# Kernel optimization log

Measured on AMD Instinct MI355X. Metric: run time of the kernel, lower is better.

## Reference

```python
import jax, jax.numpy as jnp
import numpy as np

NEG_SLOPE = 0.2
BN_EPS = 1e-5


def gat_conv(x, src, dst, W, att_src, att_dst, bias):
    """PyG-style GATConv (eval mode, shared src/dst lin, self-loops already in src/dst)."""
    N = x.shape[0]
    H, C = att_src.shape
    h = (x @ W).reshape(N, H, C)                      # [N,H,C]
    a_s = jnp.sum(h * att_src[None], axis=-1)         # [N,H]
    a_d = jnp.sum(h * att_dst[None], axis=-1)         # [N,H]
    e = jax.nn.leaky_relu(a_s[src] + a_d[dst], NEG_SLOPE)   # [E,H]
    # segment softmax over edges grouped by destination node
    m = jax.ops.segment_max(e, dst, num_segments=N)   # [N,H]
    ee = jnp.exp(e - m[dst])
    denom = jax.ops.segment_sum(ee, dst, num_segments=N)
    alpha = ee / (denom[dst] + 1e-16)                 # [E,H]
    msg = h[src] * alpha[..., None]                   # [E,H,C]
    out = jax.ops.segment_sum(msg, dst, num_segments=N)  # [N,H,C]
    return out.reshape(N, H * C) + bias


def setup_inputs() -> dict:
    key = jax.random.key(0)
    ks = jax.random.split(key, 12)
    N, E, Fin, C1, H, Fout = 50000, 800000, 128, 16, 8, 40
    HC = H * C1
    x = jax.random.normal(ks[0], (N, Fin), jnp.float32)
    edge_index = jax.random.randint(ks[1], (2, E), 0, N, dtype=jnp.int32)
    W1 = jax.random.normal(ks[2], (Fin, HC), jnp.float32) / np.sqrt(Fin).astype(np.float32)
    att_src1 = jax.random.normal(ks[3], (H, C1), jnp.float32) * 0.1
    att_dst1 = jax.random.normal(ks[4], (H, C1), jnp.float32) * 0.1
    b1 = jnp.zeros((HC,), jnp.float32)
    bn_gamma = jnp.ones((HC,), jnp.float32)
    bn_beta = jnp.zeros((HC,), jnp.float32)
    bn_mean = jnp.zeros((HC,), jnp.float32)
    bn_var = jnp.ones((HC,), jnp.float32)
    W2 = jax.random.normal(ks[5], (HC, Fout), jnp.float32) / np.sqrt(HC).astype(np.float32)
    att_src2 = jax.random.normal(ks[6], (1, Fout), jnp.float32) * 0.1
    att_dst2 = jax.random.normal(ks[7], (1, Fout), jnp.float32) * 0.1
    b2 = jnp.zeros((Fout,), jnp.float32)
    return {"x": x, "edge_index": edge_index, "W1": W1, "att_src1": att_src1,
            "att_dst1": att_dst1, "b1": b1, "bn_gamma": bn_gamma, "bn_beta": bn_beta,
            "bn_mean": bn_mean, "bn_var": bn_var, "W2": W2, "att_src2": att_src2,
            "att_dst2": att_dst2, "b2": b2}


def reference(x, edge_index, W1, att_src1, att_dst1, b1, bn_gamma, bn_beta,
              bn_mean, bn_var, W2, att_src2, att_dst2, b2):
    N = x.shape[0]
    loop = jnp.arange(N, dtype=edge_index.dtype)
    src = jnp.concatenate([edge_index[0], loop])   # PyG add_self_loops=True
    dst = jnp.concatenate([edge_index[1], loop])
    h = gat_conv(x, src, dst, W1, att_src1, att_dst1, b1)
    h = (h - bn_mean) * jax.lax.rsqrt(bn_var + BN_EPS) * bn_gamma + bn_beta  # BN eval
    h = jax.nn.elu(h)
    out = gat_conv(h, src, dst, W2, att_src2, att_dst2, b2)
    return jax.nn.log_softmax(out, axis=1)
```

## Files before the change

### kernel.cpp

```cpp
#include <hip/hip_runtime.h>
#include <hip/hip_bf16.h>
#include <math.h>

#define LRELU(v) ((v) > 0.f ? (v) : 0.2f * (v))

typedef __attribute__((ext_vector_type(8))) short bf16x8;
typedef __attribute__((ext_vector_type(4))) float f32x4;

__device__ inline unsigned int f2bf(float f) {
  unsigned int u = __float_as_uint(f);
  return (u + 0x7fffu + ((u >> 16) & 1u)) >> 16;
}
__device__ inline float bf_lo(unsigned int u) { return __uint_as_float(u << 16); }
__device__ inline float bf_hi(unsigned int u) { return __uint_as_float(u & 0xffff0000u); }

__global__ __launch_bounds__(256) void wtrans_k(const float* __restrict__ W,
                                                unsigned short* __restrict__ wt)
{
  int idx = blockIdx.x * 256 + threadIdx.x;
  int k = idx >> 7, c = idx & 127;
  wt[c * 128 + k] = (unsigned short)f2bf(W[idx]);
}

#define LDA 152
__global__ __launch_bounds__(256) void gemm1_k(
    const float* __restrict__ x, const unsigned short* __restrict__ wt,
    const float* __restrict__ atts, const float* __restrict__ attd,
    unsigned short* __restrict__ h1s, float* __restrict__ as1,
    float* __restrict__ ad1, int N)
{
  __shared__ unsigned short xs[64 * LDA];
  const int t = threadIdx.x;
  const int row0 = blockIdx.x * 64;
  const int lane = t & 63, w = t >> 6;

#pragma unroll
  for (int i = 0; i < 8; ++i) {
    int idx = t + i * 256;
    int r = idx >> 5, kq = idx & 31;
    int rr = row0 + r;
    float4 v = make_float4(0.f, 0.f, 0.f, 0.f);
    if (rr < N) v = *reinterpret_cast<const float4*>(&x[(size_t)rr * 128 + kq * 4]);
    unsigned int p0 = f2bf(v.x) | (f2bf(v.y) << 16);
    unsigned int p1 = f2bf(v.z) | (f2bf(v.w) << 16);
    *reinterpret_cast<uint2*>(&xs[r * LDA + kq * 4]) = make_uint2(p0, p1);
  }
  __syncthreads();

  const int l16 = lane & 15, lhi = lane >> 4;
  const int nb0 = w * 32;
  f32x4 acc[4][2];
#pragma unroll
  for (int m = 0; m < 4; ++m)
#pragma unroll
    for (int n = 0; n < 2; ++n) acc[m][n] = (f32x4){0.f, 0.f, 0.f, 0.f};

#pragma unroll
  for (int ks = 0; ks < 4; ++ks) {
    bf16x8 bf[2];
#pragma unroll
    for (int n = 0; n < 2; ++n) {
      int col = nb0 + n * 16 + l16;
      bf[n] = *reinterpret_cast<const bf16x8*>(&wt[col * 128 + ks * 32 + 8 * lhi]);
    }
#pragma unroll
    for (int m = 0; m < 4; ++m) {
      bf16x8 af = *reinterpret_cast<const bf16x8*>(
          &xs[(m * 16 + l16) * LDA + ks * 32 + 8 * lhi]);
      acc[m][0] = __builtin_amdgcn_mfma_f32_16x16x32_bf16(af, bf[0], acc[m][0], 0, 0, 0);
      acc[m][1] = __builtin_amdgcn_mfma_f32_16x16x32_bf16(af, bf[1], acc[m][1], 0, 0, 0);
    }
  }

#pragma unroll
  for (int n = 0; n < 2; ++n) {
    int col = nb0 + n * 16 + l16;
    float av = atts[col], dv = attd[col];
    int head = w * 2 + n;
#pragma unroll
    for (int m = 0; m < 4; ++m) {
#pragma unroll
      for (int r = 0; r < 4; ++r) {
        int row = row0 + m * 16 + lhi * 4 + r;
        float v = acc[m][n][r];
        float s = v * av, d = v * dv;
        s += __shfl_xor(s, 1); s += __shfl_xor(s, 2);
        s += __shfl_xor(s, 4); s += __shfl_xor(s, 8);
        d += __shfl_xor(d, 1); d += __shfl_xor(d, 2);
        d += __shfl_xor(d, 4); d += __shfl_xor(d, 8);
        if (row < N) {
          h1s[(size_t)row * 128 + col] = (unsigned short)f2bf(v);
          if (l16 == 0) { as1[row * 8 + head] = s; ad1[row * 8 + head] = d; }
        }
      }
    }
  }
}

#define NBUK_MAX 256

__global__ __launch_bounds__(256) void bhist_k(const int* __restrict__ ei,
                                               int E, int N,
                                               int* __restrict__ bcnt, int nbuk)
{
  __shared__ int h[NBUK_MAX];
  for (int i = threadIdx.x; i < nbuk; i += 256) h[i] = 0;
  __syncthreads();
  const int Etot = E + N;
  const int base = blockIdx.x * 4096;
#pragma unroll 4
  for (int i = threadIdx.x; i < 4096; i += 256) {
    int e = base + i;
    if (e < Etot) {
      int d = (e < E) ? ei[E + e] : (e - E);
      atomicAdd(&h[d >> 8], 1);
    }
  }
  __syncthreads();
  for (int i = threadIdx.x; i < nbuk; i += 256)
    if (h[i]) atomicAdd(&bcnt[i], h[i]);
}

__global__ __launch_bounds__(256) void bscan_k(const int* __restrict__ bcnt,
                                               int* __restrict__ bbase,
                                               int* __restrict__ bpos, int nbuk)
{
  __shared__ int wsum[4], wtot[4];
  const int t = threadIdx.x, lane = t & 63, w = t >> 6;
  int v = (t < nbuk) ? bcnt[t] : 0;
  int incl = v;
#pragma unroll
  for (int off = 1; off < 64; off <<= 1) {
    int y = __shfl_up(incl, off);
    if (lane >= off) incl += y;
  }
  if (lane == 63) wtot[w] = incl;
  __syncthreads();
  if (t == 0) {
    int a = wtot[0], b = wtot[1], c = wtot[2];
    wsum[0] = 0; wsum[1] = a; wsum[2] = a + b; wsum[3] = a + b + c;
  }
  __syncthreads();
  int ex = wsum[w] + incl - v;
  if (t < nbuk) { bbase[t] = ex; bpos[t] = ex; }
  if (t == nbuk - 1) bbase[nbuk] = ex + v;
}

__global__ __launch_bounds__(256) void bscat_k(const int* __restrict__ ei,
                                               int E, int N,
                                               int* __restrict__ bpos,
                                               unsigned int* __restrict__ stg,
                                               int nbuk)
{
  __shared__ int h[NBUK_MAX], gp[NBUK_MAX], cur[NBUK_MAX];
  for (int i = threadIdx.x; i < nbuk; i += 256) { h[i] = 0; cur[i] = 0; }
  __syncthreads();
  const int Etot = E + N;
  const int base = blockIdx.x * 4096;
  int s[16], d[16];
#pragma unroll
  for (int i = 0; i < 16; ++i) {
    int e = base + i * 256 + threadIdx.x;
    if (e < Etot) {
      if (e < E) { s[i] = ei[e]; d[i] = ei[E + e]; }
      else       { s[i] = d[i] = e - E; }
      atomicAdd(&h[d[i] >> 8], 1);
    } else d[i] = -1;
  }
  __syncthreads();
  for (int i = threadIdx.x; i < nbuk; i += 256)
    gp[i] = h[i] ? atomicAdd(&bpos[i], h[i]) : 0;
  __syncthreads();
#pragma unroll
  for (int i = 0; i < 16; ++i) {
    if (d[i] >= 0) {
      int b = d[i] >> 8;
      int r = atomicAdd(&cur[b], 1);
      stg[gp[b] + r] = ((unsigned int)s[i] << 8) | (unsigned int)(d[i] & 255);
    }
  }
}

#define CCAP 4992
__global__ __launch_bounds__(512) void csr_k(const unsigned int* __restrict__ stg,
                                             const int* __restrict__ bbase,
                                             int* __restrict__ rowptr,
                                             int* __restrict__ col,
                                             int N, int nbuk)
{
  __shared__ int nh[256], nb[257], cur[256], wsum[4];
  __shared__ int cstage[CCAP];
  const int b = blockIdx.x, t = threadIdx.x;
  const int n0 = b << 8;
  const int e0 = bbase[b], e1 = bbase[b + 1], cnt = e1 - e0;
  if (t < 256) { nh[t] = 0; cur[t] = 0; }
  __syncthreads();
  for (int i = t; i < cnt; i += 512)
    atomicAdd(&nh[stg[e0 + i] & 255u], 1);
  __syncthreads();
  if (t < 256) {
    const int lane = t & 63, w = t >> 6;
    int v = nh[t], incl = v;
#pragma unroll
    for (int off = 1; off < 64; off <<= 1) {
      int y = __shfl_up(incl, off);
      if (lane >= off) incl += y;
    }
    if (lane == 63) wsum[w] = incl;
    __syncthreads();
    if (t == 0) {
      int a = wsum[0], bb = wsum[1], c = wsum[2];
      wsum[0] = 0; wsum[1] = a; wsum[2] = a + bb; wsum[3] = a + bb + c;
    }
    __syncthreads();
    int ex = wsum[w] + incl - v;
    nb[t] = ex;
    if (t == 255) nb[256] = ex + v;
  } else {
    __syncthreads();
    __syncthreads();
  }
  __syncthreads();
  const int nnodes = min(256, N - n0);
  for (int i = t; i < nnodes; i += 512) rowptr[n0 + i] = e0 + nb[i];
  if (b == nbuk - 1 && t == 0) rowptr[N] = e1;
  for (int i = t; i < cnt; i += 512) {
    unsigned int sd = stg[e0 + i];
    int li = sd & 255u;
    int p = nb[li] + atomicAdd(&cur[li], 1);
    int sv = (int)(sd >> 8);
    if (p < CCAP) cstage[p] = sv; else col[e0 + p] = sv;
  }
  __syncthreads();
  const int lim = min(cnt, CCAP);
  for (int i = t; i < lim; i += 512) col[e0 + i] = cstage[i];
}

__global__ __launch_bounds__(256) void agg1_k(
    const unsigned int* __restrict__ h1b, const float* __restrict__ as1,
    const float* __restrict__ ad1, const int* __restrict__ rowptr,
    const int* __restrict__ col, const float* __restrict__ b1,
    const float* __restrict__ gamma, const float* __restrict__ beta,
    const float* __restrict__ mean, const float* __restrict__ var,
    float* __restrict__ hmid, int N)
{
  const int wid = threadIdx.x >> 6, lane = threadIdx.x & 63;
  const int n = blockIdx.x * 4 + wid;
  if (n >= N) return;
  const int eh = lane >> 5;
  const int cl = lane & 31;
  const int h  = cl >> 2;
  const float adv = ad1[n * 8 + h];
  float den = 0.f, a0 = 0.f, a1 = 0.f, a2 = 0.f, a3 = 0.f;
  const int jb = rowptr[n], je = rowptr[n + 1];
  for (int j = jb; j < je; j += 8) {
    int s[4]; bool v[4];
#pragma unroll
    for (int q = 0; q < 4; ++q) {
      int idx = j + 2 * q + eh;
      v[q] = idx < je;
      s[q] = col[v[q] ? idx : je - 1];
    }
    float e[4];
#pragma unroll
    for (int q = 0; q < 4; ++q) e[q] = as1[s[q] * 8 + h];
    uint2 u[4];
#pragma unroll
    for (int q = 0; q < 4; ++q)
      u[q] = *reinterpret_cast<const uint2*>(&h1b[s[q] * 64 + cl * 2]);
#pragma unroll
    for (int q = 0; q < 4; ++q) {
      float p = v[q] ? __expf(LRELU(e[q] + adv)) : 0.f;
      den += p;
      a0 += p * bf_lo(u[q].x);
      a1 += p * bf_hi(u[q].x);
      a2 += p * bf_lo(u[q].y);
      a3 += p * bf_hi(u[q].y);
    }
  }
  den += __shfl_xor(den, 32);
  a0 += __shfl_xor(a0, 32);
  a1 += __shfl_xor(a1, 32);
  a2 += __shfl_xor(a2, 32);
  a3 += __shfl_xor(a3, 32);
  if (eh == 0) {
    const int c0 = cl * 4;
    float r = 1.f / (den + 1e-16f);
    float4 bb = *reinterpret_cast<const float4*>(&b1[c0]);
    float4 mm = *reinterpret_cast<const float4*>(&mean[c0]);
    float4 vv = *reinterpret_cast<const float4*>(&var[c0]);
    float4 gg = *reinterpret_cast<const float4*>(&gamma[c0]);
    float4 be = *reinterpret_cast<const float4*>(&beta[c0]);
    float o0 = a0 * r + bb.x, o1 = a1 * r + bb.y;
    float o2 = a2 * r + bb.z, o3 = a3 * r + bb.w;
    float n0 = (o0 - mm.x) * rsqrtf(vv.x + 1e-5f) * gg.x + be.x;
    float n1 = (o1 - mm.y) * rsqrtf(vv.y + 1e-5f) * gg.y + be.y;
    float n2 = (o2 - mm.z) * rsqrtf(vv.z + 1e-5f) * gg.z + be.z;
    float n3 = (o3 - mm.w) * rsqrtf(vv.w + 1e-5f) * gg.w + be.w;
    float4 o;
    o.x = n0 > 0.f ? n0 : expm1f(n0);
    o.y = n1 > 0.f ? n1 : expm1f(n1);
    o.z = n2 > 0.f ? n2 : expm1f(n2);
    o.w = n3 > 0.f ? n3 : expm1f(n3);
    *reinterpret_cast<float4*>(&hmid[n * 128 + c0]) = o;
  }
}

__global__ __launch_bounds__(256) void gemm2_k(
    const float* __restrict__ hmid, const float* __restrict__ W2,
    const float* __restrict__ atts, const float* __restrict__ attd,
    float* __restrict__ h2p, float* __restrict__ as2, float* __restrict__ ad2,
    int N)
{
  __shared__ float hm[128 * 36];
  __shared__ float w2t[40 * 36];
  const int t = threadIdx.x;
  const int n0 = blockIdx.x * 128;
  const int lane = t & 63, w = t >> 6;
  const int ng = lane >> 3, cg = lane & 7;
  const int nloc = w * 32 + ng * 4;

  float acc[4][5];
#pragma unroll
  for (int i = 0; i < 4; ++i)
#pragma unroll
    for (int j = 0; j < 5; ++j) acc[i][j] = 0.f;

  for (int kc = 0; kc < 4; ++kc) {
    __syncthreads();
#pragma unroll
    for (int i = 0; i < 4; ++i) {
      int idx = t + i * 256;
      int r = idx >> 3, kq = idx & 7;
      int rr = n0 + r;
      float4 v = make_float4(0.f, 0.f, 0.f, 0.f);
      if (rr < N)
        v = *reinterpret_cast<const float4*>(&hmid[(size_t)rr * 128 + kc * 32 + kq * 4]);
      *reinterpret_cast<float4*>(&hm[r * 36 + kq * 4]) = v;
    }
#pragma unroll
    for (int i = 0; i < 5; ++i) {
      int flat = t + i * 256;
      int c = flat >> 5, kk = flat & 31;
      w2t[c * 36 + kk] = W2[(size_t)(kc * 32 + kk) * 40 + c];
    }
    __syncthreads();
#pragma unroll
    for (int k4 = 0; k4 < 8; ++k4) {
      float hv[4][4];
#pragma unroll
      for (int i = 0; i < 4; ++i)
        *reinterpret_cast<float4*>(hv[i]) =
            *reinterpret_cast<const float4*>(&hm[(nloc + i) * 36 + k4 * 4]);
      float wv[5][4];
#pragma unroll
      for (int j = 0; j < 5; ++j)
        *reinterpret_cast<float4*>(wv[j]) =
            *reinterpret_cast<const float4*>(&w2t[(cg * 5 + j) * 36 + k4 * 4]);
#pragma unroll
      for (int i = 0; i < 4; ++i)
#pragma unroll
        for (int j = 0; j < 5; ++j)
#pragma unroll
          for (int kk = 0; kk < 4; ++kk)
            acc[i][j] += hv[i][kk] * wv[j][kk];
    }
  }

  float asv[5], adv[5];
#pragma unroll
  for (int j = 0; j < 5; ++j) { asv[j] = atts[cg * 5 + j]; adv[j] = attd[cg * 5 + j]; }
#pragma unroll
  for (int i = 0; i < 4; ++i) {
    int n = n0 + nloc + i;
    if (n >= N) continue;
    float ps = 0.f, pd = 0.f;
#pragma unroll
    for (int j = 0; j < 5; ++j) { ps += acc[i][j] * asv[j]; pd += acc[i][j] * adv[j]; }
#pragma unroll
    for (int off = 1; off < 8; off <<= 1) {
      ps += __shfl_xor(ps, off);
      pd += __shfl_xor(pd, off);
    }
#pragma unroll
    for (int j = 0; j < 5; ++j) h2p[(size_t)n * 40 + cg * 5 + j] = acc[i][j];
    if (cg == 0) { as2[n] = ps; ad2[n] = pd; }
  }
}

__global__ __launch_bounds__(256) void agg2_k(
    const float* __restrict__ h2p, const float* __restrict__ as2,
    const float* __restrict__ ad2, const int* __restrict__ rowptr,
    const int* __restrict__ col, const float* __restrict__ b2,
    float* __restrict__ out, int N)
{
  const int wid = threadIdx.x >> 6, lane = threadIdx.x & 63;
  const int n = blockIdx.x * 4 + wid;
  if (n >= N) return;
  const int eh = lane >> 5;
  const int cl = lane & 31;
  const bool actc = cl < 20;
  const int c0 = (actc ? cl : 19) * 2;
  const float adv = ad2[n];
  float den = 0.f, a0 = 0.f, a1 = 0.f;
  const int jb = rowptr[n], je = rowptr[n + 1];
  for (int j = jb; j < je; j += 8) {
    int s[4]; bool v[4];
#pragma unroll
    for (int q = 0; q < 4; ++q) {
      int idx = j + 2 * q + eh;
      v[q] = idx < je;
      s[q] = col[v[q] ? idx : je - 1];
    }
    float e[4];
#pragma unroll
    for (int q = 0; q < 4; ++q) e[q] = as2[s[q]];
    float2 f[4];
#pragma unroll
    for (int q = 0; q < 4; ++q)
      f[q] = *reinterpret_cast<const float2*>(&h2p[s[q] * 40 + c0]);
#pragma unroll
    for (int q = 0; q < 4; ++q) {
      float p = v[q] ? __expf(LRELU(e[q] + adv)) : 0.f;
      den += p;
      a0 += p * f[q].x;
      a1 += p * f[q].y;
    }
  }
  den += __shfl_xor(den, 32);
  a0 += __shfl_xor(a0, 32);
  a1 += __shfl_xor(a1, 32);
  float r = 1.f / (den + 1e-16f);
  float o0 = a0 * r + b2[c0];
  float o1 = a1 * r + b2[c0 + 1];
  const bool act = actc && (eh == 0);
  float mv = act ? fmaxf(o0, o1) : -INFINITY;
#pragma unroll
  for (int off = 1; off < 32; off <<= 1) mv = fmaxf(mv, __shfl_xor(mv, off));
  float ex = act ? (__expf(o0 - mv) + __expf(o1 - mv)) : 0.f;
#pragma unroll
  for (int off = 1; off < 32; off <<= 1) ex += __shfl_xor(ex, off);
  float ls = logf(ex);
  if (act) {
    float2 ov = make_float2(o0 - mv - ls, o1 - mv - ls);
    *reinterpret_cast<float2*>(&out[n * 40 + c0]) = ov;
  }
}

extern "C" void kernel_launch(void* const* d_in, const int* in_sizes, int n_in,
                              void* d_out, int out_size, void* d_ws,
                              size_t ws_size, hipStream_t stream)
{
  const float* x      = (const float*)d_in[0];
  const int*   ei     = (const int*)d_in[1];
  const float* W1     = (const float*)d_in[2];
  const float* att_s1 = (const float*)d_in[3];
  const float* att_d1 = (const float*)d_in[4];
  const float* b1     = (const float*)d_in[5];
  const float* gamma  = (const float*)d_in[6];
  const float* beta   = (const float*)d_in[7];
  const float* mean   = (const float*)d_in[8];
  const float* var    = (const float*)d_in[9];
  const float* W2     = (const float*)d_in[10];
  const float* att_s2 = (const float*)d_in[11];
  const float* att_d2 = (const float*)d_in[12];
  const float* b2     = (const float*)d_in[13];
  float* out = (float*)d_out;

  const int N = in_sizes[0] / 128;
  const int E = in_sizes[1] / 2;
  const int Etot = E + N;
  const int nbuk = (N + 255) >> 8;
  const int nchunk = (Etot + 4095) / 4096;

  char* ws = (char*)d_ws;
  size_t off = 0;
  auto alloc = [&](size_t bytes) -> void* {
    void* p = ws + off;
    off = (off + bytes + 255) & ~(size_t)255;
    return p;
  };
  unsigned short* h1s = (unsigned short*)alloc((size_t)N * 128 * 2);
  float* as1  = (float*)alloc((size_t)N * 8 * 4);
  float* ad1  = (float*)alloc((size_t)N * 8 * 4);
  float* hmid = (float*)alloc((size_t)N * 128 * 4);
  int* rowptr = (int*)alloc((size_t)(N + 1) * 4);
  int* col    = (int*)alloc((size_t)Etot * 4);
  unsigned int* stg = (unsigned int*)alloc((size_t)Etot * 4);
  int* bcnt   = (int*)alloc(NBUK_MAX * 4);
  int* bbase  = (int*)alloc((NBUK_MAX + 1) * 4);
  int* bpos   = (int*)alloc(NBUK_MAX * 4);
  unsigned short* wt = (unsigned short*)alloc(16384 * 2);
  float* h2p = (float*)h1s;
  float* as2 = as1;
  float* ad2 = ad1;

  hipMemsetAsync(bcnt, 0, NBUK_MAX * 4, stream);

  wtrans_k<<<64, 256, 0, stream>>>(W1, wt);
  gemm1_k<<<(N + 63) / 64, 256, 0, stream>>>(x, wt, att_s1, att_d1,
                                             h1s, as1, ad1, N);
  bhist_k<<<nchunk, 256, 0, stream>>>(ei, E, N, bcnt, nbuk);
  bscan_k<<<1, 256, 0, stream>>>(bcnt, bbase, bpos, nbuk);
  bscat_k<<<nchunk, 256, 0, stream>>>(ei, E, N, bpos, stg, nbuk);
  csr_k<<<nbuk, 512, 0, stream>>>(stg, bbase, rowptr, col, N, nbuk);

  agg1_k<<<(N + 3) / 4, 256, 0, stream>>>((const unsigned int*)h1s, as1, ad1,
                                          rowptr, col, b1,
                                          gamma, beta, mean, var, hmid, N);
  gemm2_k<<<(N + 127) / 128, 256, 0, stream>>>(hmid, W2, att_s2, att_d2,
                                               h2p, as2, ad2, N);
  agg2_k<<<(N + 3) / 4, 256, 0, stream>>>(h2p, as2, ad2, rowptr, col, b2,
                                          out, N);
}
```

Measured before the change: 167.4 us.

## Fuse layer-2 linear projection into layer-1 aggregation kernel

Merges the first-layer attention aggregation with BN/ELU and the second-layer 128x40 projection into one kernel, keeping each node's 128-wide hidden row in shared memory instead of writing and re-reading a full hmid buffer. Each 4-node block stages all of W2 into LDS and computes the projection with a per-wave dot-product and shuffle reduction. This removes one kernel launch and a large global round-trip, but adds per-block W2 loads and more LDS use, and output buffers can no longer alias the layer-1 buffers.

```diff
diff --git a/kernel.cpp b/kernel.cpp
--- a/kernel.cpp
+++ b/kernel.cpp
@@ -236,155 +236,118 @@
   for (int i = t; i < lim; i += 512) col[e0 + i] = cstage[i];
 }
 
-__global__ __launch_bounds__(256) void agg1_k(
+__global__ __launch_bounds__(256) void agg1f_k(
     const unsigned int* __restrict__ h1b, const float* __restrict__ as1,
     const float* __restrict__ ad1, const int* __restrict__ rowptr,
     const int* __restrict__ col, const float* __restrict__ b1,
     const float* __restrict__ gamma, const float* __restrict__ beta,
     const float* __restrict__ mean, const float* __restrict__ var,
-    float* __restrict__ hmid, int N)
-{
-  const int wid = threadIdx.x >> 6, lane = threadIdx.x & 63;
-  const int n = blockIdx.x * 4 + wid;
-  if (n >= N) return;
-  const int eh = lane >> 5;
-  const int cl = lane & 31;
-  const int h  = cl >> 2;
-  const float adv = ad1[n * 8 + h];
-  float den = 0.f, a0 = 0.f, a1 = 0.f, a2 = 0.f, a3 = 0.f;
-  const int jb = rowptr[n], je = rowptr[n + 1];
-  for (int j = jb; j < je; j += 8) {
-    int s[4]; bool v[4];
-#pragma unroll
-    for (int q = 0; q < 4; ++q) {
-      int idx = j + 2 * q + eh;
-      v[q] = idx < je;
-      s[q] = col[v[q] ? idx : je - 1];
-    }
-    float e[4];
-#pragma unroll
-    for (int q = 0; q < 4; ++q) e[q] = as1[s[q] * 8 + h];
-    uint2 u[4];
-#pragma unroll
-    for (int q = 0; q < 4; ++q)
-      u[q] = *reinterpret_cast<const uint2*>(&h1b[s[q] * 64 + cl * 2]);
-#pragma unroll
-    for (int q = 0; q < 4; ++q) {
-      float p = v[q] ? __expf(LRELU(e[q] + adv)) : 0.f;
-      den += p;
-      a0 += p * bf_lo(u[q].x);
-      a1 += p * bf_hi(u[q].x);
-      a2 += p * bf_lo(u[q].y);
-      a3 += p * bf_hi(u[q].y);
-    }
-  }
-  den += __shfl_xor(den, 32);
-  a0 += __shfl_xor(a0, 32);
-  a1 += __shfl_xor(a1, 32);
-  a2 += __shfl_xor(a2, 32);
-  a3 += __shfl_xor(a3, 32);
-  if (eh == 0) {
-    const int c0 = cl * 4;
-    float r = 1.f / (den + 1e-16f);
-    float4 bb = *reinterpret_cast<const float4*>(&b1[c0]);
-    float4 mm = *reinterpret_cast<const float4*>(&mean[c0]);
-    float4 vv = *reinterpret_cast<const float4*>(&var[c0]);
-    float4 gg = *reinterpret_cast<const float4*>(&gamma[c0]);
-    float4 be = *reinterpret_cast<const float4*>(&beta[c0]);
-    float o0 = a0 * r + bb.x, o1 = a1 * r + bb.y;
-    float o2 = a2 * r + bb.z, o3 = a3 * r + bb.w;
-    float n0 = (o0 - mm.x) * rsqrtf(vv.x + 1e-5f) * gg.x + be.x;
-    float n1 = (o1 - mm.y) * rsqrtf(vv.y + 1e-5f) * gg.y + be.y;
-    float n2 = (o2 - mm.z) * rsqrtf(vv.z + 1e-5f) * gg.z + be.z;
-    float n3 = (o3 - mm.w) * rsqrtf(vv.w + 1e-5f) * gg.w + be.w;
-    float4 o;
-    o.x = n0 > 0.f ? n0 : expm1f(n0);
-    o.y = n1 > 0.f ? n1 : expm1f(n1);
-    o.z = n2 > 0.f ? n2 : expm1f(n2);
-    o.w = n3 > 0.f ? n3 : expm1f(n3);
-    *reinterpret_cast<float4*>(&hmid[n * 128 + c0]) = o;
-  }
-}
-
-__global__ __launch_bounds__(256) void gemm2_k(
-    const float* __restrict__ hmid, const float* __restrict__ W2,
-    const float* __restrict__ atts, const float* __restrict__ attd,
+    const float* __restrict__ W2, const float* __restrict__ atts2,
+    const float* __restrict__ attd2,
     float* __restrict__ h2p, float* __restrict__ as2, float* __restrict__ ad2,
     int N)
 {
-  __shared__ float hm[128 * 36];
-  __shared__ float w2t[40 * 36];
+  __shared__ float w2s[128 * 40];
+  __shared__ float hm[4 * 128];
   const int t = threadIdx.x;
-  const int n0 = blockIdx.x * 128;
-  const int lane = t & 63, w = t >> 6;
-  const int ng = lane >> 3, cg = lane & 7;
-  const int nloc = w * 32 + ng * 4;
-
-  float acc[4][5];
-#pragma unroll
-  for (int i = 0; i < 4; ++i)
-#pragma unroll
-    for (int j = 0; j < 5; ++j) acc[i][j] = 0.f;
-
-  for (int kc = 0; kc < 4; ++kc) {
-    __syncthreads();
-#pragma unroll
-    for (int i = 0; i < 4; ++i) {
-      int idx = t + i * 256;
-      int r = idx >> 3, kq = idx & 7;
-      int rr = n0 + r;
-      float4 v = make_float4(0.f, 0.f, 0.f, 0.f);
-      if (rr < N)
-        v = *reinterpret_cast<const float4*>(&hmid[(size_t)rr * 128 + kc * 32 + kq * 4]);
-      *reinterpret_cast<float4*>(&hm[r * 36 + kq * 4]) = v;
-    }
-#pragma unroll
-    for (int i = 0; i < 5; ++i) {
-      int flat = t + i * 256;
-      int c = flat >> 5, kk = flat & 31;
-      w2t[c * 36 + kk] = W2[(size_t)(kc * 32 + kk) * 40 + c];
-    }
-    __syncthreads();
-#pragma unroll
-    for (int k4 = 0; k4 < 8; ++k4) {
-      float hv[4][4];
-#pragma unroll
-      for (int i = 0; i < 4; ++i)
-        *reinterpret_cast<float4*>(hv[i]) =
-            *reinterpret_cast<const float4*>(&hm[(nloc + i) * 36 + k4 * 4]);
-      float wv[5][4];
-#pragma unroll
-      for (int j = 0; j < 5; ++j)
-        *reinterpret_cast<float4*>(wv[j]) =
-            *reinterpret_cast<const float4*>(&w2t[(cg * 5 + j) * 36 + k4 * 4]);
-#pragma unroll
-      for (int i = 0; i < 4; ++i)
-#pragma unroll
-        for (int j = 0; j < 5; ++j)
-#pragma unroll
-          for (int kk = 0; kk < 4; ++kk)
-            acc[i][j] += hv[i][kk] * wv[j][kk];
-    }
-  }
-
-  float asv[5], adv[5];
-#pragma unroll
-  for (int j = 0; j < 5; ++j) { asv[j] = atts[cg * 5 + j]; adv[j] = attd[cg * 5 + j]; }
-#pragma unroll
-  for (int i = 0; i < 4; ++i) {
-    int n = n0 + nloc + i;
-    if (n >= N) continue;
-    float ps = 0.f, pd = 0.f;
-#pragma unroll
-    for (int j = 0; j < 5; ++j) { ps += acc[i][j] * asv[j]; pd += acc[i][j] * adv[j]; }
-#pragma unroll
-    for (int off = 1; off < 8; off <<= 1) {
-      ps += __shfl_xor(ps, off);
-      pd += __shfl_xor(pd, off);
-    }
-#pragma unroll
-    for (int j = 0; j < 5; ++j) h2p[(size_t)n * 40 + cg * 5 + j] = acc[i][j];
-    if (cg == 0) { as2[n] = ps; ad2[n] = pd; }
+  const int wid = t >> 6, lane = t & 63;
+  const int n = blockIdx.x * 4 + wid;
+  const bool valid = n < N;
+
+  for (int i = t; i < 128 * 40; i += 256) w2s[i] = W2[i];
+
+  if (valid) {
+    const int eh = lane >> 5;
+    const int cl = lane & 31;
+    const int h  = cl >> 2;
+    const int c0 = cl * 4;
+    const float adv = ad1[n * 8 + h];
+    float den = 0.f, a0 = 0.f, a1 = 0.f, a2 = 0.f, a3 = 0.f;
+    const int jb = rowptr[n], je = rowptr[n + 1];
+    for (int j = jb; j < je; j += 8) {
+      int s[4]; bool v[4];
+#pragma unroll
+      for (int q = 0; q < 4; ++q) {
+        int idx = j + 2 * q + eh;
+        v[q] = idx < je;
+        s[q] = col[v[q] ? idx : je - 1];
+      }
+      float e[4];
+#pragma unroll
+      for (int q = 0; q < 4; ++q) e[q] = as1[s[q] * 8 + h];
+      uint2 u[4];
+#pragma unroll
+      for (int q = 0; q < 4; ++q)
+        u[q] = *reinterpret_cast<const uint2*>(&h1b[s[q] * 64 + cl * 2]);
+#pragma unroll
+      for (int q = 0; q < 4; ++q) {
+        float p = v[q] ? __expf(LRELU(e[q] + adv)) : 0.f;
+        den += p;
+        a0 += p * bf_lo(u[q].x);
+        a1 += p * bf_hi(u[q].x);
+        a2 += p * bf_lo(u[q].y);
+        a3 += p * bf_hi(u[q].y);
+      }
+    }
+    den += __shfl_xor(den, 32);
+    a0 += __shfl_xor(a0, 32);
+    a1 += __shfl_xor(a1, 32);
+    a2 += __shfl_xor(a2, 32);
+    a3 += __shfl_xor(a3, 32);
+    if (eh == 0) {
+      float r = 1.f / (den + 1e-16f);
+      float4 bb = *reinterpret_cast<const float4*>(&b1[c0]);
+      float4 mm = *reinterpret_cast<const float4*>(&mean[c0]);
+      float4 vv = *reinterpret_cast<const float4*>(&var[c0]);
+      float4 gg = *reinterpret_cast<const float4*>(&gamma[c0]);
+      float4 be = *reinterpret_cast<const float4*>(&beta[c0]);
+      float o0 = a0 * r + bb.x, o1 = a1 * r + bb.y;
+      float o2 = a2 * r + bb.z, o3 = a3 * r + bb.w;
+      float n0 = (o0 - mm.x) * rsqrtf(vv.x + 1e-5f) * gg.x + be.x;
+      float n1 = (o1 - mm.y) * rsqrtf(vv.y + 1e-5f) * gg.y + be.y;
+      float n2 = (o2 - mm.z) * rsqrtf(vv.z + 1e-5f) * gg.z + be.z;
+      float n3 = (o3 - mm.w) * rsqrtf(vv.w + 1e-5f) * gg.w + be.w;
+      float4 o;
+      o.x = n0 > 0.f ? n0 : expm1f(n0);
+      o.y = n1 > 0.f ? n1 : expm1f(n1);
+      o.z = n2 > 0.f ? n2 : expm1f(n2);
+      o.w = n3 > 0.f ? n3 : expm1f(n3);
+      *reinterpret_cast<float4*>(&hm[wid * 128 + c0]) = o;
+    }
+  }
+  __syncthreads();
+
+  if (valid) {
+    const int kg = lane >> 3;
+    const int cg = lane & 7;
+    float acc5[5] = {0.f, 0.f, 0.f, 0.f, 0.f};
+#pragma unroll
+    for (int j = 0; j < 16; ++j) {
+      int k = kg * 16 + j;
+      float hmv = hm[wid * 128 + k];
+      const float* wr = &w2s[k * 40 + cg * 5];
+#pragma unroll
+      for (int jc = 0; jc < 5; ++jc) acc5[jc] += hmv * wr[jc];
+    }
+#pragma unroll
+    for (int jc = 0; jc < 5; ++jc) {
+      acc5[jc] += __shfl_xor(acc5[jc], 8);
+      acc5[jc] += __shfl_xor(acc5[jc], 16);
+      acc5[jc] += __shfl_xor(acc5[jc], 32);
+    }
+    if (kg == 0) {
+      float ps = 0.f, pd = 0.f;
+#pragma unroll
+      for (int jc = 0; jc < 5; ++jc) {
+        int c = cg * 5 + jc;
+        h2p[n * 40 + c] = acc5[jc];
+        ps += acc5[jc] * atts2[c];
+        pd += acc5[jc] * attd2[c];
+      }
+      ps += __shfl_xor(ps, 1); ps += __shfl_xor(ps, 2); ps += __shfl_xor(ps, 4);
+      pd += __shfl_xor(pd, 1); pd += __shfl_xor(pd, 2); pd += __shfl_xor(pd, 4);
+      if (cg == 0) { as2[n] = ps; ad2[n] = pd; }
+    }
   }
 }
 
@@ -483,7 +446,9 @@
   unsigned short* h1s = (unsigned short*)alloc((size_t)N * 128 * 2);
   float* as1  = (float*)alloc((size_t)N * 8 * 4);
   float* ad1  = (float*)alloc((size_t)N * 8 * 4);
-  float* hmid = (float*)alloc((size_t)N * 128 * 4);
+  float* h2p  = (float*)alloc((size_t)N * 40 * 4);
+  float* as2  = (float*)alloc((size_t)N * 4);
+  float* ad2  = (float*)alloc((size_t)N * 4);
   int* rowptr = (int*)alloc((size_t)(N + 1) * 4);
   int* col    = (int*)alloc((size_t)Etot * 4);
   unsigned int* stg = (unsigned int*)alloc((size_t)Etot * 4);
@@ -491,9 +456,6 @@
   int* bbase  = (int*)alloc((NBUK_MAX + 1) * 4);
   int* bpos   = (int*)alloc(NBUK_MAX * 4);
   unsigned short* wt = (unsigned short*)alloc(16384 * 2);
-  float* h2p = (float*)h1s;
-  float* as2 = as1;
-  float* ad2 = ad1;
 
   hipMemsetAsync(bcnt, 0, NBUK_MAX * 4, stream);
 
@@ -505,11 +467,11 @@
   bscat_k<<<nchunk, 256, 0, stream>>>(ei, E, N, bpos, stg, nbuk);
   csr_k<<<nbuk, 512, 0, stream>>>(stg, bbase, rowptr, col, N, nbuk);
 
-  agg1_k<<<(N + 3) / 4, 256, 0, stream>>>((const unsigned int*)h1s, as1, ad1,
-                                          rowptr, col, b1,
-                                          gamma, beta, mean, var, hmid, N);
-  gemm2_k<<<(N + 127) / 128, 256, 0, stream>>>(hmid, W2, att_s2, att_d2,
-                                               h2p, as2, ad2, N);
+  agg1f_k<<<(N + 3) / 4, 256, 0, stream>>>((const unsigned int*)h1s, as1, ad1,
+                                           rowptr, col, b1,
+                                           gamma, beta, mean, var,
+                                           W2, att_s2, att_d2,
+                                           h2p, as2, ad2, N);
   agg2_k<<<(N + 3) / 4, 256, 0, stream>>>(h2p, as2, ad2, rowptr, col, b2,
                                           out, N);
 }
```

New measurement: 199.2 us. 19.0% more time.
